# Kernel tuning notes

Measured on AMD Instinct MI355X. Metric: run time of the kernel, lower is better.

The kernel has to match this reference:

```python
import jax, jax.numpy as jnp
import numpy as np

D = 4          # subsample stride for quantized refs
R = 6          # local search radius
P = 2 * R + 1  # 13
N = P * P      # 169
C = 32         # one-hot classes
BETA = 50.0
SIG = 1.0      # gaussian kernel sigma for kernel_soft_argmax
MPR = 12       # memory_patch_R
MPP = 2 * MPR + 1  # 25
DIL_INT = 15


def bilinear_gather(img, ys, xs):
    # img (b,c,h,w); ys,xs (b,n,h,w) float pixel coords; zero padding outside.
    b, c, h, w = img.shape
    y0f = jnp.floor(ys); x0f = jnp.floor(xs)
    wy = ys - y0f; wx = xs - x0f
    y0 = y0f.astype(jnp.int32); x0 = x0f.astype(jnp.int32)
    imgf = img.reshape(b, c, h * w)

    def corner(yi, xi, wgt):
        valid = (yi >= 0) & (yi < h) & (xi >= 0) & (xi < w)
        idx = jnp.clip(yi, 0, h - 1) * w + jnp.clip(xi, 0, w - 1)  # (b,n,h,w)
        g = jax.vmap(lambda f, ix: f[:, ix])(imgf, idx)            # (b,c,n,h,w)
        return g * (wgt * valid)[:, None]

    return (corner(y0, x0, (1 - wy) * (1 - wx))
            + corner(y0, x0 + 1, (1 - wy) * wx)
            + corner(y0 + 1, x0, wy * (1 - wx))
            + corner(y0 + 1, x0 + 1, wy * wx))


def deform_im2col(img, offset):
    # img (b,c,h,w); offset (b,h,w,2) ordered (dx,dy); returns (b,c,N,h,w)
    b, c, h, w = img.shape
    n = jnp.arange(N)
    dy = (n // P - R).astype(jnp.float32)
    dx = (n % P - R).astype(jnp.float32)
    yy = jnp.arange(h, dtype=jnp.float32)[:, None]
    xx = jnp.arange(w, dtype=jnp.float32)[None, :]
    ys = yy[None, None] + offset[..., 1][:, None] + dy[None, :, None, None]
    xs = xx[None, None] + offset[..., 0][:, None] + dx[None, :, None, None]
    return bilinear_gather(img, ys, xs)


def local_corr(t, r, rad, dil):
    # SpatialCorrelationSampler(kernel_size=1, patch_size=2*rad+1, dilation_patch=dil)
    pad = rad * dil
    rp = jnp.pad(r, ((0, 0), (0, 0), (pad, pad), (pad, pad)))
    offs = jnp.arange(2 * rad + 1) * dil

    def dot(oy, ox):
        rs = jax.lax.dynamic_slice(rp, (0, 0, oy, ox), t.shape)
        return jnp.sum(t * rs, axis=1)  # (b,h,w)

    f = jax.vmap(lambda oy: jax.vmap(lambda ox: dot(oy, ox))(offs))(offs)  # (Pp,Pp,b,h,w)
    return jnp.transpose(f, (2, 0, 1, 3, 4))  # (b,Pp,Pp,h,w), axis1=dy, axis2=dx


def unfold(x, ksz, pad):
    # torch F.unfold: (b,c,h,w) -> (b,c,ksz*ksz,h*w), n = ky*ksz+kx, zero pad
    b, c, h, w = x.shape
    xp = jnp.pad(x, ((0, 0), (0, 0), (pad, pad), (pad, pad)))
    offs = jnp.arange(ksz)
    sl = jax.vmap(lambda oy: jax.vmap(
        lambda ox: jax.lax.dynamic_slice(xp, (0, 0, oy, ox), x.shape))(offs))(offs)
    return jnp.transpose(sl, (2, 3, 0, 1, 4, 5)).reshape(b, c, ksz * ksz, h * w)


def kernel_soft_argmax(corr):
    # corr (B, N, h, w): gaussian-weight then softmax(beta * .) over N
    k = jnp.arange(P, dtype=jnp.float32)
    ctr = (P - 1) / 2.0
    g = jnp.exp(-(((k[None, :] - ctr) ** 2) + ((k[:, None] - ctr) ** 2)) / (2 * SIG ** 2))
    return jax.nn.softmax(BETA * (g.reshape(1, N, 1, 1) * corr), axis=1)


def get_grid(corr):
    # corr (B, N, h, w) -> soft-argmax grid (B, h, w, 2) in normalized coords
    B, n, h, w = corr.shape
    # replicate the torch meshgrid variable swap in the original get_grid
    x_map = jnp.broadcast_to(jnp.linspace(-1.0, 1.0, w)[None, :], (h, w)).astype(jnp.float32)
    y_map = jnp.broadcast_to(jnp.linspace(-1.0, 1.0, h)[:, None], (h, w)).astype(jnp.float32)
    xg = unfold(x_map[None, None], P, R)[:, 0]  # (1,N,hw)
    yg = unfold(y_map[None, None], P, R)[:, 0]
    wgt = corr.reshape(B, n, h * w)
    wgt = wgt / jnp.sum(wgt, 1, keepdims=True)
    gx = (wgt * xg).sum(1).reshape(B, h, w, 1)
    gy = (wgt * yg).sum(1).reshape(B, h, w, 1)
    return jnp.concatenate([gx, gy], 3)


def forward(feats_r, feats_t, quantized_r, ref_index, current_ind):
    ref_list = [int(v) for v in np.asarray(ref_index)]  # static config
    cur = int(current_ind)
    nref = feats_r.shape[0]
    nsearch = len([x for x in ref_list if cur - x > DIL_INT])
    dirates = [min(4, (cur - x) // DIL_INT + 1) for x in ref_list if cur - x > DIL_INT]
    b, c, h, w = feats_t.shape

    mdy = jnp.arange(-MPR, MPR + 1, dtype=jnp.float32)
    corrs, offsets = [], []
    for si in range(nsearch):
        cc = local_corr(feats_t, feats_r[si], MPR, dirates[si])       # (b,25,25,h,w)
        cc = jax.nn.softmax(cc.reshape(b, MPP * MPP, h * w), axis=1)
        cc = cc.reshape(b, MPP, MPP, h, w)
        offx = jnp.einsum('bpqhw,q->bhw', cc, mdy)   # expectation of dx
        offy = jnp.einsum('bpqhw,p->bhw', cc, mdy)   # expectation of dy
        off = jnp.stack([offx, offy], -1) * float(dirates[si])        # (b,h,w,2)
        offsets.append(off)
        col0 = deform_im2col(feats_r[si], off)                        # (b,c,N,h,w)
        corrs.append(jnp.einsum('bchw,bcnhw->bnhw', feats_t, col0))
    for ind in range(nsearch, nref):
        corrs.append(local_corr(feats_t, feats_r[ind], R, 1).reshape(b, N, h, w))

    corr = jnp.concatenate(corrs, 0)                 # (b*nref, N, h, w)
    corr = kernel_soft_argmax(corr)
    corr = corr.reshape(b, 1, N * nref, h * w)
    grid = get_grid(corr.reshape(-1, N, h, w))       # (b*nref, h, w, 2)

    # prep: subsample ::D and one-hot single-channel label maps
    labels = quantized_r[:, :, 0, ::D, ::D]          # (nref, b, h, w)
    qr = (labels[:, :, None] == jnp.arange(C)[None, None, :, None, None]).astype(jnp.float32)

    cols = []
    for i in range(nsearch):
        cols.append(deform_im2col(qr[i], offsets[i]).reshape(b, C, N, h * w))
    for i in range(nsearch, nref):
        cols.append(unfold(qr[i], P, R))
    image_uf = jnp.concatenate(cols, 2)              # (b, C, N*nref, hw)

    out = jnp.einsum('bnl,bcnl->bcl', corr[:, 0], image_uf).reshape(b, C, h, w)
    return out, grid


def setup_inputs() -> dict:
    key = jax.random.key(0)
    k1, k2, k3 = jax.random.split(key, 3)
    feats_r = jax.random.normal(k1, (3, 1, 64, 64, 64), dtype=jnp.float32)
    feats_t = jax.random.normal(k2, (1, 64, 64, 64), dtype=jnp.float32)
    quantized_r = jax.random.randint(k3, (3, 1, 1, 256, 256), 0, C, dtype=jnp.int32)
    return {
        'feats_r': feats_r,
        'feats_t': feats_t,
        'quantized_r': quantized_r,
        'ref_index': np.arange(3),
        'current_ind': 16,
    }


def reference(feats_r, feats_t, quantized_r, ref_index, current_ind):
    return forward(feats_r, feats_t, quantized_r, ref_index, current_ind)
```

## Files before the change

### kernel.cpp

```cpp
#include <hip/hip_runtime.h>


#define NPIX 4096

__device__ __forceinline__ float pdot(float4 t0, float4 t1, float4 t2,
                                      float4 t3, float4 a, float4 b, float4 c,
                                      float4 d) {
  float s0 = 0.f, s1 = 0.f, s2 = 0.f, s3 = 0.f;
  s0 = fmaf(t0.x, a.x, s0); s1 = fmaf(t0.y, a.y, s1);
  s2 = fmaf(t0.z, a.z, s2); s3 = fmaf(t0.w, a.w, s3);
  s0 = fmaf(t1.x, b.x, s0); s1 = fmaf(t1.y, b.y, s1);
  s2 = fmaf(t1.z, b.z, s2); s3 = fmaf(t1.w, b.w, s3);
  s0 = fmaf(t2.x, c.x, s0); s1 = fmaf(t2.y, c.y, s1);
  s2 = fmaf(t2.z, c.z, s2); s3 = fmaf(t2.w, c.w, s3);
  s0 = fmaf(t3.x, d.x, s0); s1 = fmaf(t3.y, d.y, s1);
  s2 = fmaf(t3.z, d.z, s2); s3 = fmaf(t3.w, d.w, s3);
  return (s0 + s1) + (s2 + s3);
}

__device__ __forceinline__ float qdot(float4 ta, float4 tb, float4 tc,
                                      float4 td,
                                      const float* __restrict__ rbase,
                                      int tx) {
  const float4* r = (const float4*)rbase;
  float v = pdot(ta, tb, tc, td, r[tx], r[tx + 4], r[tx + 8], r[tx + 12]);
  v += __shfl_xor(v, 1);
  v += __shfl_xor(v, 2);
  return v;
}

__device__ __forceinline__ float xpose_reduce4(float p0, float p1, float p2,
                                               float p3, int tx) {
  bool o1 = tx & 1, o2 = tx & 2;
  float x01 = __shfl_xor(o1 ? p0 : p1, 1);
  float x23 = __shfl_xor(o1 ? p2 : p3, 1);
  float sA = (o1 ? p1 : p0) + x01;
  float sB = (o1 ? p3 : p2) + x23;
  float z = __shfl_xor(o2 ? sA : sB, 2);
  return o2 ? (sB + z) : (sA + z);
}

__global__ __launch_bounds__(256) void k_transpose(
    const float* __restrict__ ft, const float* __restrict__ fr,
    const int* __restrict__ q, float* __restrict__ tT, float* __restrict__ rT,
    unsigned char* __restrict__ lblp) {
  __shared__ float tile[64][65];
  int img = blockIdx.y;
  int pixBase = blockIdx.x * 64;
  const float* src = (img == 0) ? ft : fr + (img - 1) * (64 * NPIX);
  float* dst = (img == 0) ? tT : rT + (img - 1) * (64 * NPIX);
  int tid = threadIdx.x;
#pragma unroll
  for (int it = 0; it < 4; ++it) {
    int idx = it * 256 + tid;
    int c = idx >> 4;
    int p4 = (idx & 15) << 2;
    float4 v = *(const float4*)&src[c * NPIX + pixBase + p4];
    tile[p4 + 0][c] = v.x;
    tile[p4 + 1][c] = v.y;
    tile[p4 + 2][c] = v.z;
    tile[p4 + 3][c] = v.w;
  }
  __syncthreads();
#pragma unroll
  for (int it = 0; it < 4; ++it) {
    int idx = it * 256 + tid;
    int p = idx >> 4;
    int c4 = (idx & 15) << 2;
    float4 v = make_float4(tile[p][c4], tile[p][c4 + 1], tile[p][c4 + 2],
                           tile[p][c4 + 3]);
    *(float4*)&dst[(pixBase + p) * 64 + c4] = v;
  }
  if (img >= 1 && tid < 64) {
    int pix = pixBase + tid;
    lblp[(img - 1) * 4096 + pix] = (unsigned char)
        q[(img - 1) * 65536 + (pix >> 6) * 1024 + (pix & 63) * 4];
  }
}

#define LOADT(N, XC)                                                       \
  const float4* tp##N = (const float4*)&tT[((y << 6) + (XC)) << 6];        \
  float4 t##N##0 = tp##N[tx], t##N##1 = tp##N[tx + 4],                     \
         t##N##2 = tp##N[tx + 8], t##N##3 = tp##N[tx + 12];

#define PH3(P, T0, T1, T2, T3)                                             \
  {                                                                        \
    float offx = offs[P][0], offy = offs[P][1];                            \
    int iy0 = y + (int)floorf(offy) - 6;                                   \
    int ix0 = x0 + 2 * (P) + (int)floorf(offx) - 6;                        \
    _Pragma("unroll 2") for (int r = 0; r < 4; ++r) {                      \
      int s = g + (r << 6);                                                \
      int a = s / 14, b = s - a * 14;                                      \
      int ry = iy0 + a, rx = ix0 + b;                                      \
      bool ok = (s < 196) & ((unsigned)ry < 64u) & ((unsigned)rx < 64u);   \
      int ryc = min(max(ry, 0), 63), rxc = min(max(rx, 0), 63);            \
      float v = qdot(T0, T1, T2, T3, &rT[(ryc * 64 + rxc) * 64], tx);      \
      v = ok ? v : 0.f;                                                    \
      if ((s < 196) && tx == 0) ccf[(P) * 196 + s] = v;                    \
    }                                                                      \
  }

__global__ __launch_bounds__(256) void k_fused(
    const float* __restrict__ tT, const float* __restrict__ rT,
    const unsigned char* __restrict__ lblp, float* __restrict__ out,
    float* __restrict__ grid) {
  int xg = blockIdx.x, y = blockIdx.y;
  int x0 = (xg >> 1) * 8 + (xg & 1);
  int tid = threadIdx.x;
  int g = tid >> 2, tx = tid & 3;
  int w = tid >> 6, lane = tid & 63;
  __shared__ float ccf[2500];
  __shared__ float offs[4][2];
  __shared__ float bins[4][33];

  if (tid < 132) ((float*)bins)[tid] = 0.f;

  LOADT(0, x0 + 0) LOADT(1, x0 + 2) LOADT(2, x0 + 4) LOADT(3, x0 + 6)

  {
    int u = g & 31;
    int rx = x0 - 24 + 2 * u;
    bool col_ok = ((unsigned)rx < 64u) & (u < 28);
    int rx_c = min(max(rx, 0), 63);
    int colB = rx_c * 64 + tx * 4;
    int ox = u - tx;
    bool st_col = (unsigned)ox < 25u;
    int oy = g >> 5;
    int ry = y + 2 * oy - 24;
    int ry_c = min(max(ry, 0), 63);
    const float4* rp = (const float4*)&rT[ry_c * 4096 + colB];
    float4 ra = rp[0], rb = rp[4], rc = rp[8], rd = rp[12];
#pragma unroll 1
    for (int r = 0; r < 13; ++r) {
      int ry_n = ry + 4;
      int ryn_c = min(max(ry_n, 0), 63);
      const float4* np = (const float4*)&rT[ryn_c * 4096 + colB];
      float4 na = np[0], nb = np[4], nc = np[8], nd = np[12];
      float p0 = pdot(t00, t01, t02, t03, ra, rb, rc, rd);
      float p1 = pdot(t10, t11, t12, t13, ra, rb, rc, rd);
      float p2 = pdot(t20, t21, t22, t23, ra, rb, rc, rd);
      float p3 = pdot(t30, t31, t32, t33, ra, rb, rc, rd);
      float v = xpose_reduce4(p0, p1, p2, p3, tx);
      bool ok = col_ok & (oy < 25) & ((unsigned)ry < 64u);
      v = ok ? v : 0.f;
      if (st_col && (oy < 25)) ccf[tx * 625 + oy * 25 + ox] = v;
      oy += 2;
      ry = ry_n;
      ra = na; rb = nb; rc = nc; rd = nd;
    }
  }
  __syncthreads();

  {
    float vv[10];
    float lmax = -3e38f;
#pragma unroll
    for (int it = 0; it < 10; ++it) {
      int o = lane + it * 64;
      float v = (o < 625) ? ccf[w * 625 + o] : -3e38f;
      vv[it] = v;
      lmax = fmaxf(lmax, v);
    }
#pragma unroll
    for (int o = 32; o; o >>= 1) lmax = fmaxf(lmax, __shfl_down(lmax, o));
    float m = __shfl(lmax, 0);
    float s = 0.f, sx = 0.f, sy = 0.f;
#pragma unroll
    for (int it = 0; it < 10; ++it) {
      int o = lane + it * 64;
      int oy = o / 25, ox = o - oy * 25;
      float e = __expf(vv[it] - m);
      s += e;
      sx += e * (float)(ox - 12);
      sy += e * (float)(oy - 12);
    }
#pragma unroll
    for (int o = 32; o; o >>= 1) {
      s += __shfl_down(s, o);
      sx += __shfl_down(sx, o);
      sy += __shfl_down(sy, o);
    }
    if (lane == 0) {
      offs[w][0] = 2.f * sx / s;
      offs[w][1] = 2.f * sy / s;
    }
  }
  __syncthreads();

  PH3(0, t00, t01, t02, t03)
  PH3(1, t10, t11, t12, t13)
  PH3(2, t20, t21, t22, t23)
  PH3(3, t30, t31, t32, t33)
  __syncthreads();

  {
    int px = x0 + 2 * w;
    int pix = y * 64 + px;
    float offx = offs[w][0], offy = offs[w][1];
    float fy = floorf(offy), fx = floorf(offx);
    float wy = offy - fy, wx = offx - fx;
    float w00 = (1.f - wy) * (1.f - wx), w01 = (1.f - wy) * wx;
    float w10 = wy * (1.f - wx), w11 = wy * wx;
    const float* Dw = &ccf[w * 196];
    float sc[3];
    float lmax = -3e38f;
#pragma unroll
    for (int it = 0; it < 3; ++it) {
      int o = lane + it * 64;
      float scv = -3e38f;
      if (o < 169) {
        int i = o / 13, j = o - i * 13;
        float v = w00 * Dw[i * 14 + j] + w01 * Dw[i * 14 + j + 1] +
                  w10 * Dw[(i + 1) * 14 + j] + w11 * Dw[(i + 1) * 14 + j + 1];
        float di = (float)((i - 6) * (i - 6) + (j - 6) * (j - 6));
        scv = 50.f * __expf(-0.5f * di) * v;
      }
      sc[it] = scv;
      lmax = fmaxf(lmax, scv);
    }
#pragma unroll
    for (int o = 32; o; o >>= 1) lmax = fmaxf(lmax, __shfl_down(lmax, o));
    float m = __shfl(lmax, 0);
    float ee[3];
    float s = 0.f, gx = 0.f, gy = 0.f;
#pragma unroll
    for (int it = 0; it < 3; ++it) {
      int o = lane + it * 64;
      int i = o / 13, j = o - i * 13;
      float e = __expf(sc[it] - m);
      ee[it] = e;
      int yy = y + i - 6, xx = px + j - 6;
      bool inb = (o < 169) && (unsigned)yy < 64u && (unsigned)xx < 64u;
      float xgv = inb ? (-1.f + (2.f / 63.f) * (float)xx) : 0.f;
      float ygv = inb ? (-1.f + (2.f / 63.f) * (float)yy) : 0.f;
      s += e;
      gx += e * xgv;
      gy += e * ygv;
    }
#pragma unroll
    for (int o = 32; o; o >>= 1) {
      s += __shfl_down(s, o);
      gx += __shfl_down(gx, o);
      gy += __shfl_down(gy, o);
    }
    float S = __shfl(s, 0);
    float invS = 1.f / S;
#pragma unroll
    for (int it = 0; it < 3; ++it) {
      int o = lane + it * 64;
      if (o < 169) ccf[1024 + w * 169 + o] = ee[it] * invS;
    }
    if (lane == 0) {
      grid[pix * 2 + 0] = gx * invS;
      grid[pix * 2 + 1] = gy * invS;
    }
  }
  __syncthreads();

  {
#pragma unroll 1
    for (int s = tid; s < 784; s += 256) {
      int p = s / 196, m2 = s - p * 196;
      int a = m2 / 14, b = m2 - a * 14;
      float offx = offs[p][0], offy = offs[p][1];
      float fy = floorf(offy), fx = floorf(offx);
      float wy = offy - fy, wx = offx - fx;
      int ry = y + (int)fy - 6 + a;
      int rx = x0 + 2 * p + (int)fx - 6 + b;
      if ((unsigned)ry < 64u && (unsigned)rx < 64u) {
        float w00 = (1.f - wy) * (1.f - wx), w01 = (1.f - wy) * wx;
        float w10 = wy * (1.f - wx), w11 = wy * wx;
        const float* crp = &ccf[1024 + p * 169];
        float wgt = 0.f;
        if (a < 13) {
          if (b < 13) wgt = fmaf(w00, crp[a * 13 + b], wgt);
          if (b > 0) wgt = fmaf(w01, crp[a * 13 + b - 1], wgt);
        }
        if (a > 0) {
          if (b < 13) wgt = fmaf(w10, crp[(a - 1) * 13 + b], wgt);
          if (b > 0) wgt = fmaf(w11, crp[(a - 1) * 13 + b - 1], wgt);
        }
        if (wgt != 0.f) atomicAdd(&bins[p][lblp[ry * 64 + rx]], wgt);
      }
    }
  }

  for (int k = 1; k <= 2; ++k) {
    __syncthreads();
    const float* rb0 = rT + k * (64 * NPIX);
    {
#pragma unroll 2
      for (int r = 0; r < 4; ++r) {
        int tu = g + (r << 6);
        int i = tu / 19, u = tu - i * 19;
        int ry = y + i - 6, rx = x0 - 6 + u;
        bool ok = (i < 13) & ((unsigned)ry < 64u) & ((unsigned)rx < 64u);
        int ryc = min(max(ry, 0), 63), rxc = min(max(rx, 0), 63);
        const float4* rp = (const float4*)&rb0[(ryc * 64 + rxc) * 64 + tx * 4];
        float4 ra = rp[0], rb = rp[4], rc = rp[8], rd = rp[12];
        float p0 = pdot(t00, t01, t02, t03, ra, rb, rc, rd);
        float p1 = pdot(t10, t11, t12, t13, ra, rb, rc, rd);
        float p2 = pdot(t20, t21, t22, t23, ra, rb, rc, rd);
        float p3 = pdot(t30, t31, t32, t33, ra, rb, rc, rd);
        float v = xpose_reduce4(p0, p1, p2, p3, tx);
        v = ok ? v : 0.f;
        int j = u - 2 * tx;
        if ((i < 13) && ((unsigned)j < 13u)) ccf[tx * 169 + i * 13 + j] = v;
      }
    }
    __syncthreads();
    {
      int px = x0 + 2 * w;
      int pix = y * 64 + px;
      float sc[3];
      float lmax = -3e38f;
#pragma unroll
      for (int it = 0; it < 3; ++it) {
        int o = lane + it * 64;
        float scv = -3e38f;
        if (o < 169) {
          int i = o / 13, j = o - i * 13;
          float di = (float)((i - 6) * (i - 6) + (j - 6) * (j - 6));
          scv = 50.f * __expf(-0.5f * di) * ccf[w * 169 + o];
        }
        sc[it] = scv;
        lmax = fmaxf(lmax, scv);
      }
#pragma unroll
      for (int o = 32; o; o >>= 1) lmax = fmaxf(lmax, __shfl_down(lmax, o));
      float m = __shfl(lmax, 0);
      float ee[3];
      float s = 0.f, gx = 0.f, gy = 0.f;
#pragma unroll
      for (int it = 0; it < 3; ++it) {
        int o = lane + it * 64;
        int i = o / 13, j = o - i * 13;
        float e = __expf(sc[it] - m);
        ee[it] = e;
        int yy = y + i - 6, xx = px + j - 6;
        bool inb = (o < 169) && (unsigned)yy < 64u && (unsigned)xx < 64u;
        float xgv = inb ? (-1.f + (2.f / 63.f) * (float)xx) : 0.f;
        float ygv = inb ? (-1.f + (2.f / 63.f) * (float)yy) : 0.f;
        s += e;
        gx += e * xgv;
        gy += e * ygv;
      }
#pragma unroll
      for (int o = 32; o; o >>= 1) {
        s += __shfl_down(s, o);
        gx += __shfl_down(gx, o);
        gy += __shfl_down(gy, o);
      }
      float S = __shfl(s, 0);
      float invS = 1.f / S;
#pragma unroll
      for (int it = 0; it < 3; ++it) {
        int o = lane + it * 64;
        if (o < 169) {
          int i = o / 13, j = o - i * 13;
          int yy = y + i - 6, xx = px + j - 6;
          if ((unsigned)yy < 64u && (unsigned)xx < 64u)
            atomicAdd(&bins[w][lblp[(k << 12) + yy * 64 + xx]],
                      ee[it] * invS);
        }
      }
      if (lane == 0) {
        grid[(k * NPIX + pix) * 2 + 0] = gx * invS;
        grid[(k * NPIX + pix) * 2 + 1] = gy * invS;
      }
    }
  }
  __syncthreads();

  if (tid < 128) {
    int p = tid & 3, c = tid >> 2;
    out[c * NPIX + y * 64 + x0 + 2 * p] = bins[p][c];
  }
}

extern "C" void kernel_launch(void* const* d_in, const int* in_sizes, int n_in,
                              void* d_out, int out_size, void* d_ws,
                              size_t ws_size, hipStream_t stream) {
  const float* fr = (const float*)d_in[0];
  const float* ft = (const float*)d_in[1];
  const int* q = (const int*)d_in[2];
  float* out = (float*)d_out;
  float* grid = out + 32 * NPIX;

  float* ws = (float*)d_ws;
  float* tT = ws;
  float* rT = ws + 262144;
  unsigned char* lblp = (unsigned char*)(ws + 1048576);

  k_transpose<<<dim3(64, 4), 256, 0, stream>>>(ft, fr, q, tT, rT, lblp);
  k_fused<<<dim3(16, 64), 256, 0, stream>>>(tT, rT, lblp, out, grid);
}
```

Measured before the change: 58.96 us.

## Double block to 512 threads, split softmax across wave pairs, stage target in LDS

Raises the fused kernel block size from 256 to 512 threads so each pixel's work is split across two wavefronts. The softmax reductions are merged across the pair through shared memory using an online max/sum rescale. Target feature vectors move from registers to LDS to cut register pressure. The loops drop their manual software prefetch, and extra __syncthreads are added for the cross-wave merges. The aim is more parallelism and occupancy, at the cost of more synchronization and LDS reads.

```diff
diff --git a/kernel.cpp b/kernel.cpp
--- a/kernel.cpp
+++ b/kernel.cpp
@@ -18,17 +18,6 @@
   return (s0 + s1) + (s2 + s3);
 }
 
-__device__ __forceinline__ float qdot(float4 ta, float4 tb, float4 tc,
-                                      float4 td,
-                                      const float* __restrict__ rbase,
-                                      int tx) {
-  const float4* r = (const float4*)rbase;
-  float v = pdot(ta, tb, tc, td, r[tx], r[tx + 4], r[tx + 8], r[tx + 12]);
-  v += __shfl_xor(v, 1);
-  v += __shfl_xor(v, 2);
-  return v;
-}
-
 __device__ __forceinline__ float xpose_reduce4(float p0, float p1, float p2,
                                                float p3, int tx) {
   bool o1 = tx & 1, o2 = tx & 2;
@@ -38,6 +27,17 @@
   float sB = (o1 ? p3 : p2) + x23;
   float z = __shfl_xor(o2 ? sA : sB, 2);
   return o2 ? (sB + z) : (sA + z);
+}
+
+__device__ __forceinline__ float wredmax(float v) {
+#pragma unroll
+  for (int o = 32; o; o >>= 1) v = fmaxf(v, __shfl_down(v, o));
+  return __shfl(v, 0);
+}
+__device__ __forceinline__ float wredsum(float v) {
+#pragma unroll
+  for (int o = 32; o; o >>= 1) v += __shfl_down(v, o);
+  return __shfl(v, 0);
 }
 
 __global__ __launch_bounds__(256) void k_transpose(
@@ -78,135 +78,140 @@
   }
 }
 
-#define LOADT(N, XC)                                                       \
-  const float4* tp##N = (const float4*)&tT[((y << 6) + (XC)) << 6];        \
-  float4 t##N##0 = tp##N[tx], t##N##1 = tp##N[tx + 4],                     \
-         t##N##2 = tp##N[tx + 8], t##N##3 = tp##N[tx + 12];
-
-#define PH3(P, T0, T1, T2, T3)                                             \
-  {                                                                        \
-    float offx = offs[P][0], offy = offs[P][1];                            \
-    int iy0 = y + (int)floorf(offy) - 6;                                   \
-    int ix0 = x0 + 2 * (P) + (int)floorf(offx) - 6;                        \
-    _Pragma("unroll 2") for (int r = 0; r < 4; ++r) {                      \
-      int s = g + (r << 6);                                                \
-      int a = s / 14, b = s - a * 14;                                      \
-      int ry = iy0 + a, rx = ix0 + b;                                      \
-      bool ok = (s < 196) & ((unsigned)ry < 64u) & ((unsigned)rx < 64u);   \
-      int ryc = min(max(ry, 0), 63), rxc = min(max(rx, 0), 63);            \
-      float v = qdot(T0, T1, T2, T3, &rT[(ryc * 64 + rxc) * 64], tx);      \
-      v = ok ? v : 0.f;                                                    \
-      if ((s < 196) && tx == 0) ccf[(P) * 196 + s] = v;                    \
-    }                                                                      \
-  }
-
-__global__ __launch_bounds__(256) void k_fused(
+__global__ __launch_bounds__(512) void k_fused(
     const float* __restrict__ tT, const float* __restrict__ rT,
     const unsigned char* __restrict__ lblp, float* __restrict__ out,
     float* __restrict__ grid) {
   int xg = blockIdx.x, y = blockIdx.y;
   int x0 = (xg >> 1) * 8 + (xg & 1);
   int tid = threadIdx.x;
-  int g = tid >> 2, tx = tid & 3;
+  int gg = tid >> 2, tx = tid & 3;
   int w = tid >> 6, lane = tid & 63;
+  int p = w & 3, h = w >> 2;
+
+  __shared__ __align__(16) float tlds[4][64];
   __shared__ float ccf[2500];
   __shared__ float offs[4][2];
   __shared__ float bins[4][33];
+  __shared__ float wred[8][4];
 
   if (tid < 132) ((float*)bins)[tid] = 0.f;
-
-  LOADT(0, x0 + 0) LOADT(1, x0 + 2) LOADT(2, x0 + 4) LOADT(3, x0 + 6)
+  if (tid < 64) {
+    int pp = tid >> 4, c4 = tid & 15;
+    ((float4*)&tlds[pp][0])[c4] =
+        ((const float4*)&tT[((y << 6) + x0 + 2 * pp) << 6])[c4];
+  }
+  __syncthreads();
+
+  const float4* TL0 = (const float4*)&tlds[0][0];
+  const float4* TL1 = (const float4*)&tlds[1][0];
+  const float4* TL2 = (const float4*)&tlds[2][0];
+  const float4* TL3 = (const float4*)&tlds[3][0];
 
   {
-    int u = g & 31;
+    int u = gg & 31;
     int rx = x0 - 24 + 2 * u;
     bool col_ok = ((unsigned)rx < 64u) & (u < 28);
-    int rx_c = min(max(rx, 0), 63);
-    int colB = rx_c * 64 + tx * 4;
+    int colB = min(max(rx, 0), 63) * 64 + tx * 4;
     int ox = u - tx;
     bool st_col = (unsigned)ox < 25u;
-    int oy = g >> 5;
-    int ry = y + 2 * oy - 24;
-    int ry_c = min(max(ry, 0), 63);
-    const float4* rp = (const float4*)&rT[ry_c * 4096 + colB];
-    float4 ra = rp[0], rb = rp[4], rc = rp[8], rd = rp[12];
+    int oyb = gg >> 5;
 #pragma unroll 1
-    for (int r = 0; r < 13; ++r) {
-      int ry_n = ry + 4;
-      int ryn_c = min(max(ry_n, 0), 63);
-      const float4* np = (const float4*)&rT[ryn_c * 4096 + colB];
-      float4 na = np[0], nb = np[4], nc = np[8], nd = np[12];
-      float p0 = pdot(t00, t01, t02, t03, ra, rb, rc, rd);
-      float p1 = pdot(t10, t11, t12, t13, ra, rb, rc, rd);
-      float p2 = pdot(t20, t21, t22, t23, ra, rb, rc, rd);
-      float p3 = pdot(t30, t31, t32, t33, ra, rb, rc, rd);
+    for (int r = 0; r < 7; ++r) {
+      int oy = oyb + 4 * r;
+      int ry = y + 2 * oy - 24;
+      bool ok = col_ok & (oy < 25) & ((unsigned)ry < 64u);
+      const float4* rp = (const float4*)&rT[min(max(ry, 0), 63) * 4096 + colB];
+      float4 ra = rp[0], rb = rp[4], rc = rp[8], rd = rp[12];
+      float p0 = pdot(TL0[tx], TL0[tx + 4], TL0[tx + 8], TL0[tx + 12], ra, rb, rc, rd);
+      float p1 = pdot(TL1[tx], TL1[tx + 4], TL1[tx + 8], TL1[tx + 12], ra, rb, rc, rd);
+      float p2 = pdot(TL2[tx], TL2[tx + 4], TL2[tx + 8], TL2[tx + 12], ra, rb, rc, rd);
+      float p3 = pdot(TL3[tx], TL3[tx + 4], TL3[tx + 8], TL3[tx + 12], ra, rb, rc, rd);
       float v = xpose_reduce4(p0, p1, p2, p3, tx);
-      bool ok = col_ok & (oy < 25) & ((unsigned)ry < 64u);
       v = ok ? v : 0.f;
       if (st_col && (oy < 25)) ccf[tx * 625 + oy * 25 + ox] = v;
-      oy += 2;
-      ry = ry_n;
-      ra = na; rb = nb; rc = nc; rd = nd;
     }
   }
   __syncthreads();
 
   {
-    float vv[10];
-    float lmax = -3e38f;
-#pragma unroll
-    for (int it = 0; it < 10; ++it) {
-      int o = lane + it * 64;
-      float v = (o < 625) ? ccf[w * 625 + o] : -3e38f;
+    float vv[5];
+    float m = -3e38f;
+#pragma unroll
+    for (int it = 0; it < 5; ++it) {
+      int o = lane + (h << 6) + (it << 7);
+      float v = (o < 625) ? ccf[p * 625 + o] : -3e38f;
       vv[it] = v;
-      lmax = fmaxf(lmax, v);
-    }
-#pragma unroll
-    for (int o = 32; o; o >>= 1) lmax = fmaxf(lmax, __shfl_down(lmax, o));
-    float m = __shfl(lmax, 0);
+      m = fmaxf(m, v);
+    }
+    m = wredmax(m);
     float s = 0.f, sx = 0.f, sy = 0.f;
 #pragma unroll
-    for (int it = 0; it < 10; ++it) {
-      int o = lane + it * 64;
+    for (int it = 0; it < 5; ++it) {
+      int o = lane + (h << 6) + (it << 7);
       int oy = o / 25, ox = o - oy * 25;
       float e = __expf(vv[it] - m);
       s += e;
       sx += e * (float)(ox - 12);
       sy += e * (float)(oy - 12);
     }
-#pragma unroll
-    for (int o = 32; o; o >>= 1) {
-      s += __shfl_down(s, o);
-      sx += __shfl_down(sx, o);
-      sy += __shfl_down(sy, o);
-    }
+    s = wredsum(s); sx = wredsum(sx); sy = wredsum(sy);
     if (lane == 0) {
-      offs[w][0] = 2.f * sx / s;
-      offs[w][1] = 2.f * sy / s;
-    }
-  }
-  __syncthreads();
-
-  PH3(0, t00, t01, t02, t03)
-  PH3(1, t10, t11, t12, t13)
-  PH3(2, t20, t21, t22, t23)
-  PH3(3, t30, t31, t32, t33)
+      wred[w][0] = m; wred[w][1] = s; wred[w][2] = sx; wred[w][3] = sy;
+    }
+    __syncthreads();
+    if (h == 0 && lane == 0) {
+      float m2 = wred[w + 4][0], s2 = wred[w + 4][1];
+      float sx2 = wred[w + 4][2], sy2 = wred[w + 4][3];
+      float M = fmaxf(m, m2);
+      float f1 = __expf(m - M), f2 = __expf(m2 - M);
+      float S = s * f1 + s2 * f2;
+      offs[p][0] = 2.f * (sx * f1 + sx2 * f2) / S;
+      offs[p][1] = 2.f * (sy * f1 + sy2 * f2) / S;
+    }
+  }
   __syncthreads();
 
   {
-    int px = x0 + 2 * w;
+    int pp = gg >> 5;
+    float offx = offs[pp][0], offy = offs[pp][1];
+    int iy0 = y + (int)floorf(offy) - 6;
+    int ix0 = x0 + 2 * pp + (int)floorf(offx) - 6;
+    const float4* TL = (const float4*)&tlds[pp][0];
+    float4 T0 = TL[tx], T1 = TL[tx + 4], T2 = TL[tx + 8], T3 = TL[tx + 12];
+    int ib = gg & 31;
+#pragma unroll 1
+    for (int r = 0; r < 7; ++r) {
+      int idx = ib + (r << 5);
+      int a = idx / 14, b = idx - a * 14;
+      int ry = iy0 + a, rx = ix0 + b;
+      bool ok = (idx < 196) & ((unsigned)ry < 64u) & ((unsigned)rx < 64u);
+      const float4* rp = (const float4*)
+          &rT[(min(max(ry, 0), 63) * 64 + min(max(rx, 0), 63)) * 64];
+      float4 ra = rp[tx], rb = rp[tx + 4], rc = rp[tx + 8], rd = rp[tx + 12];
+      float v = pdot(T0, T1, T2, T3, ra, rb, rc, rd);
+      v += __shfl_xor(v, 1);
+      v += __shfl_xor(v, 2);
+      v = ok ? v : 0.f;
+      if ((idx < 196) && tx == 0) ccf[pp * 196 + idx] = v;
+    }
+  }
+  __syncthreads();
+
+  {
+    int px = x0 + 2 * p;
     int pix = y * 64 + px;
-    float offx = offs[w][0], offy = offs[w][1];
+    float offx = offs[p][0], offy = offs[p][1];
     float fy = floorf(offy), fx = floorf(offx);
     float wy = offy - fy, wx = offx - fx;
     float w00 = (1.f - wy) * (1.f - wx), w01 = (1.f - wy) * wx;
     float w10 = wy * (1.f - wx), w11 = wy * wx;
-    const float* Dw = &ccf[w * 196];
-    float sc[3];
-    float lmax = -3e38f;
-#pragma unroll
-    for (int it = 0; it < 3; ++it) {
-      int o = lane + it * 64;
+    const float* Dw = &ccf[p * 196];
+    float sc[2];
+    float m = -3e38f;
+#pragma unroll
+    for (int it = 0; it < 2; ++it) {
+      int o = lane + (h << 6) + (it << 7);
       float scv = -3e38f;
       if (o < 169) {
         int i = o / 13, j = o - i * 13;
@@ -216,16 +221,14 @@
         scv = 50.f * __expf(-0.5f * di) * v;
       }
       sc[it] = scv;
-      lmax = fmaxf(lmax, scv);
-    }
-#pragma unroll
-    for (int o = 32; o; o >>= 1) lmax = fmaxf(lmax, __shfl_down(lmax, o));
-    float m = __shfl(lmax, 0);
-    float ee[3];
+      m = fmaxf(m, scv);
+    }
+    m = wredmax(m);
+    float ee[2];
     float s = 0.f, gx = 0.f, gy = 0.f;
 #pragma unroll
-    for (int it = 0; it < 3; ++it) {
-      int o = lane + it * 64;
+    for (int it = 0; it < 2; ++it) {
+      int o = lane + (h << 6) + (it << 7);
       int i = o / 13, j = o - i * 13;
       float e = __expf(sc[it] - m);
       ee[it] = e;
@@ -237,71 +240,75 @@
       gx += e * xgv;
       gy += e * ygv;
     }
-#pragma unroll
-    for (int o = 32; o; o >>= 1) {
-      s += __shfl_down(s, o);
-      gx += __shfl_down(gx, o);
-      gy += __shfl_down(gy, o);
-    }
-    float S = __shfl(s, 0);
-    float invS = 1.f / S;
-#pragma unroll
-    for (int it = 0; it < 3; ++it) {
-      int o = lane + it * 64;
-      if (o < 169) ccf[1024 + w * 169 + o] = ee[it] * invS;
-    }
+    s = wredsum(s); gx = wredsum(gx); gy = wredsum(gy);
     if (lane == 0) {
-      grid[pix * 2 + 0] = gx * invS;
-      grid[pix * 2 + 1] = gy * invS;
+      wred[w][0] = m; wred[w][1] = s; wred[w][2] = gx; wred[w][3] = gy;
+    }
+    __syncthreads();
+    float mo = wred[w ^ 4][0], so = wred[w ^ 4][1];
+    float gxo = wred[w ^ 4][2], gyo = wred[w ^ 4][3];
+    float M = fmaxf(m, mo);
+    float fs = __expf(m - M), fo = __expf(mo - M);
+    float invS = 1.f / (s * fs + so * fo);
+#pragma unroll
+    for (int it = 0; it < 2; ++it) {
+      int o = lane + (h << 6) + (it << 7);
+      if (o < 169) ccf[1024 + p * 169 + o] = ee[it] * fs * invS;
+    }
+    if (h == 0 && lane == 0) {
+      grid[pix * 2 + 0] = (gx * fs + gxo * fo) * invS;
+      grid[pix * 2 + 1] = (gy * fs + gyo * fo) * invS;
     }
   }
   __syncthreads();
 
   {
+    float offx = offs[p][0], offy = offs[p][1];
+    float fy = floorf(offy), fx = floorf(offx);
+    float wy = offy - fy, wx = offx - fx;
+    float w00 = (1.f - wy) * (1.f - wx), w01 = (1.f - wy) * wx;
+    float w10 = wy * (1.f - wx), w11 = wy * wx;
+    int by = y + (int)fy - 6, bx = x0 + 2 * p + (int)fx - 6;
+    const float* crp = &ccf[1024 + p * 169];
+#pragma unroll
+    for (int it = 0; it < 2; ++it) {
+      int idx = lane + (h << 6) + (it << 7);
+      if (idx < 196) {
+        int a = idx / 14, b = idx - a * 14;
+        int ry = by + a, rx = bx + b;
+        if ((unsigned)ry < 64u && (unsigned)rx < 64u) {
+          float wgt = 0.f;
+          if (a < 13) {
+            if (b < 13) wgt = fmaf(w00, crp[a * 13 + b], wgt);
+            if (b > 0) wgt = fmaf(w01, crp[a * 13 + b - 1], wgt);
+          }
+          if (a > 0) {
+            if (b < 13) wgt = fmaf(w10, crp[(a - 1) * 13 + b], wgt);
+            if (b > 0) wgt = fmaf(w11, crp[(a - 1) * 13 + b - 1], wgt);
+          }
+          if (wgt != 0.f) atomicAdd(&bins[p][lblp[ry * 64 + rx]], wgt);
+        }
+      }
+    }
+  }
+
 #pragma unroll 1
-    for (int s = tid; s < 784; s += 256) {
-      int p = s / 196, m2 = s - p * 196;
-      int a = m2 / 14, b = m2 - a * 14;
-      float offx = offs[p][0], offy = offs[p][1];
-      float fy = floorf(offy), fx = floorf(offx);
-      float wy = offy - fy, wx = offx - fx;
-      int ry = y + (int)fy - 6 + a;
-      int rx = x0 + 2 * p + (int)fx - 6 + b;
-      if ((unsigned)ry < 64u && (unsigned)rx < 64u) {
-        float w00 = (1.f - wy) * (1.f - wx), w01 = (1.f - wy) * wx;
-        float w10 = wy * (1.f - wx), w11 = wy * wx;
-        const float* crp = &ccf[1024 + p * 169];
-        float wgt = 0.f;
-        if (a < 13) {
-          if (b < 13) wgt = fmaf(w00, crp[a * 13 + b], wgt);
-          if (b > 0) wgt = fmaf(w01, crp[a * 13 + b - 1], wgt);
-        }
-        if (a > 0) {
-          if (b < 13) wgt = fmaf(w10, crp[(a - 1) * 13 + b], wgt);
-          if (b > 0) wgt = fmaf(w11, crp[(a - 1) * 13 + b - 1], wgt);
-        }
-        if (wgt != 0.f) atomicAdd(&bins[p][lblp[ry * 64 + rx]], wgt);
-      }
-    }
-  }
-
   for (int k = 1; k <= 2; ++k) {
-    __syncthreads();
     const float* rb0 = rT + k * (64 * NPIX);
     {
-#pragma unroll 2
-      for (int r = 0; r < 4; ++r) {
-        int tu = g + (r << 6);
+#pragma unroll 1
+      for (int r = 0; r < 2; ++r) {
+        int tu = gg + (r << 7);
         int i = tu / 19, u = tu - i * 19;
         int ry = y + i - 6, rx = x0 - 6 + u;
         bool ok = (i < 13) & ((unsigned)ry < 64u) & ((unsigned)rx < 64u);
-        int ryc = min(max(ry, 0), 63), rxc = min(max(rx, 0), 63);
-        const float4* rp = (const float4*)&rb0[(ryc * 64 + rxc) * 64 + tx * 4];
-        float4 ra = rp[0], rb = rp[4], rc = rp[8], rd = rp[12];
-        float p0 = pdot(t00, t01, t02, t03, ra, rb, rc, rd);
-        float p1 = pdot(t10, t11, t12, t13, ra, rb, rc, rd);
-        float p2 = pdot(t20, t21, t22, t23, ra, rb, rc, rd);
-        float p3 = pdot(t30, t31, t32, t33, ra, rb, rc, rd);
+        const float4* rp = (const float4*)
+            &rb0[(min(max(ry, 0), 63) * 64 + min(max(rx, 0), 63)) * 64];
+        float4 ra = rp[tx], rb = rp[tx + 4], rc = rp[tx + 8], rd = rp[tx + 12];
+        float p0 = pdot(TL0[tx], TL0[tx + 4], TL0[tx + 8], TL0[tx + 12], ra, rb, rc, rd);
+        float p1 = pdot(TL1[tx], TL1[tx + 4], TL1[tx + 8], TL1[tx + 12], ra, rb, rc, rd);
+        float p2 = pdot(TL2[tx], TL2[tx + 4], TL2[tx + 8], TL2[tx + 12], ra, rb, rc, rd);
+        float p3 = pdot(TL3[tx], TL3[tx + 4], TL3[tx + 8], TL3[tx + 12], ra, rb, rc, rd);
         float v = xpose_reduce4(p0, p1, p2, p3, tx);
         v = ok ? v : 0.f;
         int j = u - 2 * tx;
@@ -310,30 +317,28 @@
     }
     __syncthreads();
     {
-      int px = x0 + 2 * w;
+      int px = x0 + 2 * p;
       int pix = y * 64 + px;
-      float sc[3];
-      float lmax = -3e38f;
-#pragma unroll
-      for (int it = 0; it < 3; ++it) {
-        int o = lane + it * 64;
+      float sc[2];
+      float m = -3e38f;
+#pragma unroll
+      for (int it = 0; it < 2; ++it) {
+        int o = lane + (h << 6) + (it << 7);
         float scv = -3e38f;
         if (o < 169) {
           int i = o / 13, j = o - i * 13;
           float di = (float)((i - 6) * (i - 6) + (j - 6) * (j - 6));
-          scv = 50.f * __expf(-0.5f * di) * ccf[w * 169 + o];
+          scv = 50.f * __expf(-0.5f * di) * ccf[p * 169 + o];
         }
         sc[it] = scv;
-        lmax = fmaxf(lmax, scv);
-      }
-#pragma unroll
-      for (int o = 32; o; o >>= 1) lmax = fmaxf(lmax, __shfl_down(lmax, o));
-      float m = __shfl(lmax, 0);
-      float ee[3];
+        m = fmaxf(m, scv);
+      }
+      m = wredmax(m);
+      float ee[2];
       float s = 0.f, gx = 0.f, gy = 0.f;
 #pragma unroll
-      for (int it = 0; it < 3; ++it) {
-        int o = lane + it * 64;
+      for (int it = 0; it < 2; ++it) {
+        int o = lane + (h << 6) + (it << 7);
         int i = o / 13, j = o - i * 13;
         float e = __expf(sc[it] - m);
         ee[it] = e;
@@ -345,36 +350,38 @@
         gx += e * xgv;
         gy += e * ygv;
       }
-#pragma unroll
-      for (int o = 32; o; o >>= 1) {
-        s += __shfl_down(s, o);
-        gx += __shfl_down(gx, o);
-        gy += __shfl_down(gy, o);
-      }
-      float S = __shfl(s, 0);
-      float invS = 1.f / S;
-#pragma unroll
-      for (int it = 0; it < 3; ++it) {
-        int o = lane + it * 64;
+      s = wredsum(s); gx = wredsum(gx); gy = wredsum(gy);
+      if (lane == 0) {
+        wred[w][0] = m; wred[w][1] = s; wred[w][2] = gx; wred[w][3] = gy;
+      }
+      __syncthreads();
+      float mo = wred[w ^ 4][0], so = wred[w ^ 4][1];
+      float gxo = wred[w ^ 4][2], gyo = wred[w ^ 4][3];
+      float M = fmaxf(m, mo);
+      float fs = __expf(m - M), fo = __expf(mo - M);
+      float invS = 1.f / (s * fs + so * fo);
+#pragma unroll
+      for (int it = 0; it < 2; ++it) {
+        int o = lane + (h << 6) + (it << 7);
         if (o < 169) {
           int i = o / 13, j = o - i * 13;
           int yy = y + i - 6, xx = px + j - 6;
           if ((unsigned)yy < 64u && (unsigned)xx < 64u)
-            atomicAdd(&bins[w][lblp[(k << 12) + yy * 64 + xx]],
-                      ee[it] * invS);
+            atomicAdd(&bins[p][lblp[(k << 12) + yy * 64 + xx]],
+                      ee[it] * fs * invS);
         }
       }
-      if (lane == 0) {
-        grid[(k * NPIX + pix) * 2 + 0] = gx * invS;
-        grid[(k * NPIX + pix) * 2 + 1] = gy * invS;
+      if (h == 0 && lane == 0) {
+        grid[(k * NPIX + pix) * 2 + 0] = (gx * fs + gxo * fo) * invS;
+        grid[(k * NPIX + pix) * 2 + 1] = (gy * fs + gyo * fo) * invS;
       }
     }
   }
   __syncthreads();
 
   if (tid < 128) {
-    int p = tid & 3, c = tid >> 2;
-    out[c * NPIX + y * 64 + x0 + 2 * p] = bins[p][c];
+    int pp = tid & 3, c = tid >> 2;
+    out[c * NPIX + y * 64 + x0 + 2 * pp] = bins[pp][c];
   }
 }
 
@@ -393,5 +400,5 @@
   unsigned char* lblp = (unsigned char*)(ws + 1048576);
 
   k_transpose<<<dim3(64, 4), 256, 0, stream>>>(ft, fr, q, tT, rT, lblp);
-  k_fused<<<dim3(16, 64), 256, 0, stream>>>(tT, rT, lblp, out, grid);
-}
+  k_fused<<<dim3(16, 64), 512, 0, stream>>>(tT, rT, lblp, out, grid);
+}
```

Result: faster. 55.25 us (-6.3%).
